# Performance work log

Measured on AMD Instinct MI355X. Metric: run time of the kernel, lower is better.

Reference implementation:

```python
import jax, jax.numpy as jnp
import numpy as np

N_NODES = 50000
N_EDGES = 800000
IN_DIM = 256
OUT_DIM = 64
HEADS = 4
NEG_SLOPE = 0.2  # PyG GATConv default


def setup_inputs() -> dict:
    key = jax.random.key(0)
    k_x, k_e, k_w, k_as, k_ad = jax.random.split(key, 5)
    x = jax.random.normal(k_x, (N_NODES, IN_DIM), dtype=jnp.float32)
    edge_index = jax.random.randint(k_e, (2, N_EDGES), 0, N_NODES, dtype=jnp.int64)
    # Glorot-ish scaled params (as in PyG GATConv)
    W = jax.random.normal(k_w, (IN_DIM, HEADS * OUT_DIM), dtype=jnp.float32) / np.sqrt(IN_DIM)
    att_src = jax.random.normal(k_as, (HEADS, OUT_DIM), dtype=jnp.float32) / np.sqrt(OUT_DIM)
    att_dst = jax.random.normal(k_ad, (HEADS, OUT_DIM), dtype=jnp.float32) / np.sqrt(OUT_DIM)
    bias = jnp.zeros((HEADS * OUT_DIM,), dtype=jnp.float32)
    return {"x": x, "edge_index": edge_index, "W": W,
            "att_src": att_src, "att_dst": att_dst, "bias": bias}


def reference(x, edge_index, W, att_src, att_dst, bias):
    N = x.shape[0]
    H, C = att_src.shape
    # add self-loops (PyG GATConv default add_self_loops=True)
    loop = jnp.arange(N, dtype=edge_index.dtype)
    src = jnp.concatenate([edge_index[0], loop])  # [E+N] message sources j
    dst = jnp.concatenate([edge_index[1], loop])  # [E+N] message targets i

    xh = (x @ W).reshape(N, H, C)                 # [N, H, C]
    a_src = jnp.einsum('nhc,hc->nh', xh, att_src)  # [N, H]
    a_dst = jnp.einsum('nhc,hc->nh', xh, att_dst)  # [N, H]

    logits = jax.nn.leaky_relu(a_src[src] + a_dst[dst], NEG_SLOPE)  # [E+N, H]
    # segment softmax over incoming edges of each destination node
    seg_max = jax.ops.segment_max(logits, dst, num_segments=N)      # [N, H]
    e = jnp.exp(logits - seg_max[dst])
    seg_sum = jax.ops.segment_sum(e, dst, num_segments=N)           # [N, H]
    alpha = e / seg_sum[dst]                                        # [E+N, H]

    # weighted scatter-aggregate of source features
    msgs = alpha[:, :, None] * xh[src]                              # [E+N, H, C]
    out = jax.ops.segment_sum(msgs, dst, num_segments=N)            # [N, H, C]
    out = out.reshape(N, H * C) + bias                              # concat heads + bias
    # h.dim() == 2 here, so the original's mean(dim=1) branch is not taken
    return out
```

## Files before the change

### kernel.cpp

```cpp
#include <hip/hip_runtime.h>

#define NEG_SLOPE 0.2f
#define LRELU(x) ((x) > 0.0f ? (x) : NEG_SLOPE * (x))

typedef short short8 __attribute__((ext_vector_type(8)));
typedef unsigned short ushort8 __attribute__((ext_vector_type(8)));
typedef float f32x4v __attribute__((ext_vector_type(4)));

__device__ __forceinline__ unsigned short f2bf(float f) {
  unsigned int u = __float_as_uint(f);
  unsigned int r = (u + 0x7FFFu + ((u >> 16) & 1u)) >> 16;
  return (unsigned short)r;
}

__device__ __forceinline__ float bf2f(unsigned short u) {
  return __uint_as_float(((unsigned int)u) << 16);
}

__device__ __forceinline__ void gload_lds16(const void* g, void* l) {
  __builtin_amdgcn_global_load_lds(
      (const __attribute__((address_space(1))) unsigned int*)g,
      (__attribute__((address_space(3))) unsigned int*)l, 16, 0, 0);
}

#define CBX 1536
#define CBC 512
#define CBW 64
#define CBF 512

__global__ __launch_bounds__(256) void fused_pre(
    const float* __restrict__ X, unsigned short* __restrict__ Xb,
    const float* __restrict__ W, unsigned short* __restrict__ Wtb,
    const int* __restrict__ ei, int* __restrict__ deg,
    int totalX, int validX, int E) {
  int b = blockIdx.x;
  int tid = threadIdx.x;
  if (b < CBX) {
    for (int i = (b * 256 + tid) * 4; i < totalX; i += CBX * 256 * 4) {
      ushort4 o;
      if (i < validX) {
        float4 v = *reinterpret_cast<const float4*>(X + i);
        o.x = f2bf(v.x); o.y = f2bf(v.y); o.z = f2bf(v.z); o.w = f2bf(v.w);
      } else {
        o.x = o.y = o.z = o.w = 0;
      }
      *reinterpret_cast<ushort4*>(Xb + i) = o;
    }
  } else if (b < CBX + CBC) {
    int bb = b - CBX;
    for (int e = bb * 256 + tid; e < E; e += CBC * 256)
      atomicAdd(&deg[ei[E + e]], 1);
  } else {
    int bb = b - CBX - CBC;
    for (int idx = bb * 256 + tid; idx < 256 * 256; idx += CBW * 256) {
      int n = idx >> 8, k = idx & 255;
      Wtb[n * 256 + k] = f2bf(W[k * 256 + n]);
    }
  }
}

__global__ __launch_bounds__(1024) void scan1_kernel(const int* __restrict__ deg,
                                                     int* __restrict__ row_start,
                                                     int* __restrict__ bsum, int N) {
  __shared__ int buf[1024];
  int i = blockIdx.x * 1024 + (int)threadIdx.x;
  int v = (i < N) ? deg[i] : 0;
  buf[threadIdx.x] = v;
  __syncthreads();
  int run = v;
  for (int off = 1; off < 1024; off <<= 1) {
    int t = ((int)threadIdx.x >= off) ? buf[threadIdx.x - off] : 0;
    __syncthreads();
    run += t;
    buf[threadIdx.x] = run;
    __syncthreads();
  }
  if (i < N) row_start[i] = run - v;
  if (threadIdx.x == 1023) bsum[blockIdx.x] = run;
}

__global__ __launch_bounds__(1024) void scan_off(int* __restrict__ row_start,
                                                 const int* __restrict__ bsum,
                                                 int nb, int N) {
  __shared__ int s_off;
  int b = blockIdx.x;
  if (threadIdx.x < 64) {
    int acc = 0;
    for (int j = (int)threadIdx.x; j < b; j += 64) acc += bsum[j];
    for (int off = 32; off; off >>= 1) acc += __shfl_down(acc, off, 64);
    if (threadIdx.x == 0) s_off = acc;
  }
  __syncthreads();
  int off = s_off;
  int i = b * 1024 + (int)threadIdx.x;
  if (i < N) row_start[i] += off;
  if (b == nb - 1 && threadIdx.x == 0) row_start[N] = off + bsum[b];
}

__global__ __launch_bounds__(256) void fused_main(
    const unsigned short* __restrict__ Xb, const unsigned short* __restrict__ Wtb,
    const float* __restrict__ attS, const float* __restrict__ attD,
    unsigned short* __restrict__ XHb, float* __restrict__ a_src,
    float* __restrict__ a_dst,
    const int* __restrict__ ei, const int* __restrict__ row_start,
    int* __restrict__ cursor, int* __restrict__ csr_src,
    int nGemm, int E, int N) {
  __shared__ unsigned short lA[128 * 32];
  __shared__ unsigned short lB[128 * 32];
  const int bid = blockIdx.x;
  const int tid = threadIdx.x;

  if (bid >= nGemm) {
    int bb = bid - nGemm;
    for (int e = bb * 256 + tid; e < E; e += CBF * 256) {
      int d = ei[E + e];
      int slot = row_start[d] + atomicAdd(&cursor[d], 1);
      csr_src[slot] = ei[e];
    }
    return;
  }

  const int lane = tid & 63;
  const int wave = tid >> 6;
  const int n0 = (bid & 1) * 128;
  const int m0 = (bid >> 1) * 128;
  const int wr = (wave >> 1) * 64;
  const int wc = (wave & 1) * 64;

  f32x4v acc[4][4];
#pragma unroll
  for (int i = 0; i < 4; ++i)
#pragma unroll
    for (int j = 0; j < 4; ++j) acc[i][j] = (f32x4v)(0.0f);

  const int srow = tid >> 2;
  const int skb = (tid & 3) * 16;
  const char* XbC = (const char*)Xb;
  const char* WtC = (const char*)Wtb;
  char* lAc = (char*)&lA[0];
  char* lBc = (char*)&lB[0];
  const int ldsB0 = wave * 1024;
  const int lr = lane & 15;
  const int hq = lane >> 4;
  const int kq = hq * 16;

  for (int k0 = 0; k0 < 256; k0 += 32) {
    const size_t kbyte = (size_t)k0 * 2 + skb;
    gload_lds16(XbC + (size_t)(m0 + srow) * 512 + kbyte, lAc + ldsB0);
    gload_lds16(XbC + (size_t)(m0 + srow + 64) * 512 + kbyte, lAc + ldsB0 + 4096);
    gload_lds16(WtC + (size_t)(n0 + srow) * 512 + kbyte, lBc + ldsB0);
    gload_lds16(WtC + (size_t)(n0 + srow + 64) * 512 + kbyte, lBc + ldsB0 + 4096);
    __syncthreads();

    short8 a[4], b[4];
#pragma unroll
    for (int i = 0; i < 4; ++i)
      a[i] = *reinterpret_cast<const short8*>(lAc + (wr + i * 16 + lr) * 64 + kq);
#pragma unroll
    for (int j = 0; j < 4; ++j)
      b[j] = *reinterpret_cast<const short8*>(lBc + (wc + j * 16 + lr) * 64 + kq);
#pragma unroll
    for (int i = 0; i < 4; ++i)
#pragma unroll
      for (int j = 0; j < 4; ++j)
        acc[i][j] = __builtin_amdgcn_mfma_f32_16x16x32_bf16(a[i], b[j], acc[i][j], 0, 0, 0);
    __syncthreads();
  }

  const int h = (n0 + wc) >> 6;
  float ws_[4], wd_[4];
#pragma unroll
  for (int j = 0; j < 4; ++j) {
    ws_[j] = attS[h * 64 + j * 16 + lr];
    wd_[j] = attD[h * 64 + j * 16 + lr];
  }
  const int rbase = m0 + wr + hq * 4;

#pragma unroll
  for (int i = 0; i < 4; ++i) {
#pragma unroll
    for (int r = 0; r < 4; ++r) {
      float ps = 0.f, pd = 0.f;
#pragma unroll
      for (int j = 0; j < 4; ++j) {
        ps += acc[i][j][r] * ws_[j];
        pd += acc[i][j][r] * wd_[j];
      }
#pragma unroll
      for (int off = 1; off < 16; off <<= 1) {
        ps += __shfl_xor(ps, off, 64);
        pd += __shfl_xor(pd, off, 64);
      }
      int row = rbase + i * 16 + r;
      if (lr == 0 && row < N) {
        a_src[row * 4 + h] = ps;
        a_dst[row * 4 + h] = pd;
      }
    }
  }

#pragma unroll
  for (int i = 0; i < 4; ++i)
#pragma unroll
    for (int j = 0; j < 4; ++j) {
      int col = n0 + wc + j * 16 + lr;
#pragma unroll
      for (int r = 0; r < 4; ++r)
        XHb[(size_t)(rbase + i * 16 + r) * 256 + col] = f2bf(acc[i][j][r]);
    }
}

__global__ __launch_bounds__(256) void gat_agg(
    const unsigned short* __restrict__ XHb, const float* __restrict__ a_src,
    const float* __restrict__ a_dst, const int* __restrict__ row_start,
    const int* __restrict__ csr_src, const float* __restrict__ bias,
    float* __restrict__ out, int N) {
  int wid = threadIdx.x >> 6;
  int lane = threadIdx.x & 63;
  int node = blockIdx.x * 4 + wid;
  if (node >= N) return;

  const int half = lane >> 5;
  const int l5 = lane & 31;
  const int h = l5 >> 3;
  const int c = l5 << 3;
  const unsigned short* __restrict__ xrow = XHb + c;

  float ad_h = a_dst[node * 4 + h];
  float as_h = a_src[node * 4 + h];

  int start = row_start[node];
  int end = row_start[node + 1];

  float acc[8];
  float sw = 0.f;
  if (half == 0) {
    float wself = __expf(LRELU(as_h + ad_h));
    ushort8 sv = *reinterpret_cast<const ushort8*>(xrow + (size_t)node * 256);
#pragma unroll
    for (int k = 0; k < 8; ++k) acc[k] = wself * bf2f(sv[k]);
    sw = wself;
  } else {
#pragma unroll
    for (int k = 0; k < 8; ++k) acc[k] = 0.f;
  }

  int p = start;
  for (; p + 8 <= end; p += 8) {
    int s0 = csr_src[p + half];
    int s1 = csr_src[p + 2 + half];
    int s2 = csr_src[p + 4 + half];
    int s3 = csr_src[p + 6 + half];
    float a0 = a_src[s0 * 4 + h] + ad_h;
    float a1 = a_src[s1 * 4 + h] + ad_h;
    float a2 = a_src[s2 * 4 + h] + ad_h;
    float a3 = a_src[s3 * 4 + h] + ad_h;
    ushort8 u0 = *reinterpret_cast<const ushort8*>(xrow + (size_t)s0 * 256);
    ushort8 u1 = *reinterpret_cast<const ushort8*>(xrow + (size_t)s1 * 256);
    ushort8 u2 = *reinterpret_cast<const ushort8*>(xrow + (size_t)s2 * 256);
    ushort8 u3 = *reinterpret_cast<const ushort8*>(xrow + (size_t)s3 * 256);
    float w0 = __expf(LRELU(a0));
    float w1 = __expf(LRELU(a1));
    float w2 = __expf(LRELU(a2));
    float w3 = __expf(LRELU(a3));
#pragma unroll
    for (int k = 0; k < 8; ++k) {
      acc[k] += w0 * bf2f(u0[k]);
      acc[k] += w1 * bf2f(u1[k]);
      acc[k] += w2 * bf2f(u2[k]);
      acc[k] += w3 * bf2f(u3[k]);
    }
    sw += (w0 + w1) + (w2 + w3);
  }
#pragma unroll
  for (int k = 0; k < 4; ++k) {
    int idx = p + 2 * k + half;
    if (idx < end) {
      int s = csr_src[idx];
      float aa = a_src[s * 4 + h] + ad_h;
      ushort8 u = *reinterpret_cast<const ushort8*>(xrow + (size_t)s * 256);
      float ww = __expf(LRELU(aa));
#pragma unroll
      for (int q = 0; q < 8; ++q) acc[q] += ww * bf2f(u[q]);
      sw += ww;
    }
  }

  sw += __shfl_xor(sw, 32, 64);
#pragma unroll
  for (int k = 0; k < 8; ++k) acc[k] += __shfl_xor(acc[k], 32, 64);

  if (half == 0) {
    float inv = 1.0f / sw;
    float4 b0 = *reinterpret_cast<const float4*>(bias + c);
    float4 b1 = *reinterpret_cast<const float4*>(bias + c + 4);
    float4 o0, o1;
    o0.x = acc[0] * inv + b0.x; o0.y = acc[1] * inv + b0.y;
    o0.z = acc[2] * inv + b0.z; o0.w = acc[3] * inv + b0.w;
    o1.x = acc[4] * inv + b1.x; o1.y = acc[5] * inv + b1.y;
    o1.z = acc[6] * inv + b1.z; o1.w = acc[7] * inv + b1.w;
    *reinterpret_cast<float4*>(out + (size_t)node * 256 + c) = o0;
    *reinterpret_cast<float4*>(out + (size_t)node * 256 + c + 4) = o1;
  }
}

extern "C" void kernel_launch(void* const* d_in, const int* in_sizes, int n_in,
                              void* d_out, int out_size, void* d_ws, size_t ws_size,
                              hipStream_t stream) {
  const float* x    = (const float*)d_in[0];
  const int*   ei   = (const int*)d_in[1];
  const float* Wm   = (const float*)d_in[2];
  const float* attS = (const float*)d_in[3];
  const float* attD = (const float*)d_in[4];
  const float* bias = (const float*)d_in[5];
  float* out = (float*)d_out;

  const int N = in_sizes[0] / 256;
  const int E = in_sizes[1] / 2;
  const int Mp = (N + 127) / 128 * 128;
  const int nb = (N + 1023) / 1024;

  char* w = (char*)d_ws;
  unsigned short* XHb = (unsigned short*)w;  w += (size_t)Mp * 256 * 2;
  unsigned short* Xb  = (unsigned short*)w;  w += (size_t)Mp * 256 * 2;
  unsigned short* Wtb = (unsigned short*)w;  w += (size_t)256 * 256 * 2;
  float* a_src = (float*)w;                  w += (size_t)N * 4 * 4;
  float* a_dst = (float*)w;                  w += (size_t)N * 4 * 4;
  int* deg = (int*)w;                        w += (size_t)N * 4;
  int* cursor = (int*)w;                     w += (size_t)N * 4;
  int* row_start = (int*)w;                  w += ((size_t)(N + 1) * 4 + 255) / 256 * 256;
  int* bsum = (int*)w;                       w += ((size_t)nb * 4 + 255) / 256 * 256;
  int* csr_src = (int*)w;                    w += (size_t)E * 4;

  hipMemsetAsync(deg, 0, (size_t)2 * N * 4, stream);

  fused_pre<<<CBX + CBC + CBW, 256, 0, stream>>>(x, Xb, Wm, Wtb, ei, deg,
                                                 Mp * 256, N * 256, E);

  scan1_kernel<<<nb, 1024, 0, stream>>>(deg, row_start, bsum, N);
  scan_off<<<nb, 1024, 0, stream>>>(row_start, bsum, nb, N);

  const int nGemm = 2 * (Mp / 128);
  fused_main<<<nGemm + CBF, 256, 0, stream>>>(Xb, Wtb, attS, attD, XHb, a_src, a_dst,
                                              ei, row_start, cursor, csr_src,
                                              nGemm, E, N);

  gat_agg<<<(N + 3) / 4, 256, 0, stream>>>(XHb, a_src, a_dst, row_start, csr_src,
                                           bias, out, N);
}
```

Measured before the change: 173.3 us.

## Fuse fp32-to-bf16 conversion of X into GEMM A-tile loads, retile 64x256

Drops the separate pre-pass that converted X to a bf16 workspace buffer. The GEMM now reads fp32 X directly, converts it in registers with packed bf16 conversion, and writes it to LDS, prefetching the next K slice in registers. Tiles change from 128x128 to 64 rows by full 256 columns, so each X row is read once instead of twice. This removes one full write and re-read of X, at the cost of register-path A loads and a larger B tile per block.

```diff
diff --git a/kernel.cpp b/kernel.cpp
--- a/kernel.cpp
+++ b/kernel.cpp
@@ -17,41 +17,32 @@
   return __uint_as_float(((unsigned int)u) << 16);
 }
 
+__device__ __forceinline__ unsigned int cvt_pk_bf16(float lo, float hi) {
+  unsigned int r;
+  asm("v_cvt_pk_bf16_f32 %0, %1, %2" : "=v"(r) : "v"(lo), "v"(hi));
+  return r;
+}
+
 __device__ __forceinline__ void gload_lds16(const void* g, void* l) {
   __builtin_amdgcn_global_load_lds(
       (const __attribute__((address_space(1))) unsigned int*)g,
       (__attribute__((address_space(3))) unsigned int*)l, 16, 0, 0);
 }
 
-#define CBX 1536
-#define CBC 512
+#define CBC 448
 #define CBW 64
 #define CBF 512
 
 __global__ __launch_bounds__(256) void fused_pre(
-    const float* __restrict__ X, unsigned short* __restrict__ Xb,
     const float* __restrict__ W, unsigned short* __restrict__ Wtb,
-    const int* __restrict__ ei, int* __restrict__ deg,
-    int totalX, int validX, int E) {
+    const int* __restrict__ ei, int* __restrict__ deg, int E) {
   int b = blockIdx.x;
   int tid = threadIdx.x;
-  if (b < CBX) {
-    for (int i = (b * 256 + tid) * 4; i < totalX; i += CBX * 256 * 4) {
-      ushort4 o;
-      if (i < validX) {
-        float4 v = *reinterpret_cast<const float4*>(X + i);
-        o.x = f2bf(v.x); o.y = f2bf(v.y); o.z = f2bf(v.z); o.w = f2bf(v.w);
-      } else {
-        o.x = o.y = o.z = o.w = 0;
-      }
-      *reinterpret_cast<ushort4*>(Xb + i) = o;
-    }
-  } else if (b < CBX + CBC) {
-    int bb = b - CBX;
-    for (int e = bb * 256 + tid; e < E; e += CBC * 256)
+  if (b < CBC) {
+    for (int e = b * 256 + tid; e < E; e += CBC * 256)
       atomicAdd(&deg[ei[E + e]], 1);
   } else {
-    int bb = b - CBX - CBC;
+    int bb = b - CBC;
     for (int idx = bb * 256 + tid; idx < 256 * 256; idx += CBW * 256) {
       int n = idx >> 8, k = idx & 255;
       Wtb[n * 256 + k] = f2bf(W[k * 256 + n]);
@@ -97,16 +88,16 @@
   if (b == nb - 1 && threadIdx.x == 0) row_start[N] = off + bsum[b];
 }
 
-__global__ __launch_bounds__(256) void fused_main(
-    const unsigned short* __restrict__ Xb, const unsigned short* __restrict__ Wtb,
+__global__ __launch_bounds__(256, 3) void fused_main(
+    const float* __restrict__ Xf, const unsigned short* __restrict__ Wtb,
     const float* __restrict__ attS, const float* __restrict__ attD,
     unsigned short* __restrict__ XHb, float* __restrict__ a_src,
     float* __restrict__ a_dst,
     const int* __restrict__ ei, const int* __restrict__ row_start,
     int* __restrict__ cursor, int* __restrict__ csr_src,
     int nGemm, int E, int N) {
-  __shared__ unsigned short lA[128 * 32];
-  __shared__ unsigned short lB[128 * 32];
+  __shared__ unsigned short lA[64 * 32];
+  __shared__ unsigned short lB[256 * 32];
   const int bid = blockIdx.x;
   const int tid = threadIdx.x;
 
@@ -122,92 +113,116 @@
 
   const int lane = tid & 63;
   const int wave = tid >> 6;
-  const int n0 = (bid & 1) * 128;
-  const int m0 = (bid >> 1) * 128;
-  const int wr = (wave >> 1) * 64;
+  const int m0 = bid * 64;
+  const int wrow = (wave >> 1) * 32;
   const int wc = (wave & 1) * 64;
 
-  f32x4v acc[4][4];
-#pragma unroll
-  for (int i = 0; i < 4; ++i)
-#pragma unroll
-    for (int j = 0; j < 4; ++j) acc[i][j] = (f32x4v)(0.0f);
+  f32x4v acc[2][8];
+#pragma unroll
+  for (int i = 0; i < 2; ++i)
+#pragma unroll
+    for (int j = 0; j < 8; ++j) acc[i][j] = (f32x4v)(0.0f);
 
   const int srow = tid >> 2;
   const int skb = (tid & 3) * 16;
-  const char* XbC = (const char*)Xb;
+  const int arow = tid >> 2;
+  const int acol = (tid & 3) * 8;
+  const float* aptr = Xf + (size_t)min(m0 + arow, N - 1) * 256 + acol;
+
   const char* WtC = (const char*)Wtb;
   char* lAc = (char*)&lA[0];
   char* lBc = (char*)&lB[0];
-  const int ldsB0 = wave * 1024;
+  const int ldsW = wave * 1024;
   const int lr = lane & 15;
   const int hq = lane >> 4;
-  const int kq = hq * 16;
-
-  for (int k0 = 0; k0 < 256; k0 += 32) {
-    const size_t kbyte = (size_t)k0 * 2 + skb;
-    gload_lds16(XbC + (size_t)(m0 + srow) * 512 + kbyte, lAc + ldsB0);
-    gload_lds16(XbC + (size_t)(m0 + srow + 64) * 512 + kbyte, lAc + ldsB0 + 4096);
-    gload_lds16(WtC + (size_t)(n0 + srow) * 512 + kbyte, lBc + ldsB0);
-    gload_lds16(WtC + (size_t)(n0 + srow + 64) * 512 + kbyte, lBc + ldsB0 + 4096);
+
+  float4 nv0 = *reinterpret_cast<const float4*>(aptr);
+  float4 nv1 = *reinterpret_cast<const float4*>(aptr + 4);
+
+#pragma unroll
+  for (int kk = 0; kk < 8; ++kk) {
+    const int k0 = kk * 32;
+#pragma unroll
+    for (int is = 0; is < 4; ++is)
+      gload_lds16(WtC + (size_t)(is * 64 + srow) * 512 + (size_t)k0 * 2 + skb,
+                  lBc + is * 4096 + ldsW);
+    {
+      uint4 wv;
+      wv.x = cvt_pk_bf16(nv0.x, nv0.y);
+      wv.y = cvt_pk_bf16(nv0.z, nv0.w);
+      wv.z = cvt_pk_bf16(nv1.x, nv1.y);
+      wv.w = cvt_pk_bf16(nv1.z, nv1.w);
+      *reinterpret_cast<uint4*>(lAc + arow * 64 + (tid & 3) * 16) = wv;
+    }
+    if (kk < 7) {
+      nv0 = *reinterpret_cast<const float4*>(aptr + k0 + 32);
+      nv1 = *reinterpret_cast<const float4*>(aptr + k0 + 36);
+    }
     __syncthreads();
 
-    short8 a[4], b[4];
-#pragma unroll
-    for (int i = 0; i < 4; ++i)
-      a[i] = *reinterpret_cast<const short8*>(lAc + (wr + i * 16 + lr) * 64 + kq);
-#pragma unroll
-    for (int j = 0; j < 4; ++j)
-      b[j] = *reinterpret_cast<const short8*>(lBc + (wc + j * 16 + lr) * 64 + kq);
-#pragma unroll
-    for (int i = 0; i < 4; ++i)
+    short8 a[2];
+#pragma unroll
+    for (int i = 0; i < 2; ++i)
+      a[i] = *reinterpret_cast<const short8*>(lAc + (wrow + i * 16 + lr) * 64 + hq * 16);
+#pragma unroll
+    for (int half = 0; half < 2; ++half) {
+      short8 b[4];
 #pragma unroll
       for (int j = 0; j < 4; ++j)
-        acc[i][j] = __builtin_amdgcn_mfma_f32_16x16x32_bf16(a[i], b[j], acc[i][j], 0, 0, 0);
+        b[j] = *reinterpret_cast<const short8*>(
+            lBc + (half * 128 + wc + j * 16 + lr) * 64 + hq * 16);
+#pragma unroll
+      for (int i = 0; i < 2; ++i)
+#pragma unroll
+        for (int j = 0; j < 4; ++j)
+          acc[i][half * 4 + j] =
+              __builtin_amdgcn_mfma_f32_16x16x32_bf16(a[i], b[j], acc[i][half * 4 + j], 0, 0, 0);
+    }
     __syncthreads();
   }
 
-  const int h = (n0 + wc) >> 6;
-  float ws_[4], wd_[4];
-#pragma unroll
-  for (int j = 0; j < 4; ++j) {
-    ws_[j] = attS[h * 64 + j * 16 + lr];
-    wd_[j] = attD[h * 64 + j * 16 + lr];
-  }
-  const int rbase = m0 + wr + hq * 4;
-
-#pragma unroll
-  for (int i = 0; i < 4; ++i) {
-#pragma unroll
-    for (int r = 0; r < 4; ++r) {
-      float ps = 0.f, pd = 0.f;
+  const int rbase = m0 + wrow + hq * 4;
+#pragma unroll
+  for (int half = 0; half < 2; ++half) {
+    const int h = half * 2 + (wave & 1);
+    float ws_[4], wd_[4];
+#pragma unroll
+    for (int j = 0; j < 4; ++j) {
+      ws_[j] = attS[h * 64 + j * 16 + lr];
+      wd_[j] = attD[h * 64 + j * 16 + lr];
+    }
+#pragma unroll
+    for (int i = 0; i < 2; ++i) {
+#pragma unroll
+      for (int r = 0; r < 4; ++r) {
+        float ps = 0.f, pd = 0.f;
+#pragma unroll
+        for (int j = 0; j < 4; ++j) {
+          ps += acc[i][half * 4 + j][r] * ws_[j];
+          pd += acc[i][half * 4 + j][r] * wd_[j];
+        }
+#pragma unroll
+        for (int off = 1; off < 16; off <<= 1) {
+          ps += __shfl_xor(ps, off, 64);
+          pd += __shfl_xor(pd, off, 64);
+        }
+        int row = rbase + i * 16 + r;
+        if (lr == 0 && row < N) {
+          a_src[row * 4 + h] = ps;
+          a_dst[row * 4 + h] = pd;
+        }
+      }
+    }
+#pragma unroll
+    for (int i = 0; i < 2; ++i)
 #pragma unroll
       for (int j = 0; j < 4; ++j) {
-        ps += acc[i][j][r] * ws_[j];
-        pd += acc[i][j][r] * wd_[j];
+        int col = half * 128 + wc + j * 16 + lr;
+#pragma unroll
+        for (int r = 0; r < 4; ++r)
+          XHb[(size_t)(rbase + i * 16 + r) * 256 + col] = f2bf(acc[i][half * 4 + j][r]);
       }
-#pragma unroll
-      for (int off = 1; off < 16; off <<= 1) {
-        ps += __shfl_xor(ps, off, 64);
-        pd += __shfl_xor(pd, off, 64);
-      }
-      int row = rbase + i * 16 + r;
-      if (lr == 0 && row < N) {
-        a_src[row * 4 + h] = ps;
-        a_dst[row * 4 + h] = pd;
-      }
-    }
-  }
-
-#pragma unroll
-  for (int i = 0; i < 4; ++i)
-#pragma unroll
-    for (int j = 0; j < 4; ++j) {
-      int col = n0 + wc + j * 16 + lr;
-#pragma unroll
-      for (int r = 0; r < 4; ++r)
-        XHb[(size_t)(rbase + i * 16 + r) * 256 + col] = f2bf(acc[i][j][r]);
-    }
+  }
 }
 
 __global__ __launch_bounds__(256) void gat_agg(
@@ -317,12 +332,11 @@
 
   const int N = in_sizes[0] / 256;
   const int E = in_sizes[1] / 2;
-  const int Mp = (N + 127) / 128 * 128;
+  const int Mp = (N + 63) / 64 * 64;
   const int nb = (N + 1023) / 1024;
 
   char* w = (char*)d_ws;
   unsigned short* XHb = (unsigned short*)w;  w += (size_t)Mp * 256 * 2;
-  unsigned short* Xb  = (unsigned short*)w;  w += (size_t)Mp * 256 * 2;
   unsigned short* Wtb = (unsigned short*)w;  w += (size_t)256 * 256 * 2;
   float* a_src = (float*)w;                  w += (size_t)N * 4 * 4;
   float* a_dst = (float*)w;                  w += (size_t)N * 4 * 4;
@@ -334,14 +348,13 @@
 
   hipMemsetAsync(deg, 0, (size_t)2 * N * 4, stream);
 
-  fused_pre<<<CBX + CBC + CBW, 256, 0, stream>>>(x, Xb, Wm, Wtb, ei, deg,
-                                                 Mp * 256, N * 256, E);
+  fused_pre<<<CBC + CBW, 256, 0, stream>>>(Wm, Wtb, ei, deg, E);
 
   scan1_kernel<<<nb, 1024, 0, stream>>>(deg, row_start, bsum, N);
   scan_off<<<nb, 1024, 0, stream>>>(row_start, bsum, nb, N);
 
-  const int nGemm = 2 * (Mp / 128);
-  fused_main<<<nGemm + CBF, 256, 0, stream>>>(Xb, Wtb, attS, attD, XHb, a_src, a_dst,
+  const int nGemm = Mp / 64;
+  fused_main<<<nGemm + CBF, 256, 0, stream>>>(x, Wtb, attS, attD, XHb, a_src, a_dst,
                                               ei, row_start, cursor, csr_src,
                                               nGemm, E, N);
 
```

New measurement: 167.2 us. 1.04x faster.

## Fuse fp32-to-bf16 conversion of X into the GEMM A-tile load

Applied to the files above, without the earlier changes.

Drops the separate pass that converted X to bf16 into a workspace buffer. The GEMM now reads fp32 X directly into registers, converts pairs with v_cvt_pk_bf16_f32, and writes the result to LDS, prefetching the next K slice into registers before the barrier. This removes a full write and re-read of a bf16 copy of X, plus the conversion blocks in the prologue kernel, whose degree-count block count is also cut. In exchange the GEMM reads twice as many bytes of A, clamps padded rows to the last valid row instead of zero-filling them, and uses register-staged stores rather than direct global-to-LDS loads for A.

```diff
diff --git a/kernel.cpp b/kernel.cpp
--- a/kernel.cpp
+++ b/kernel.cpp
@@ -17,41 +17,32 @@
   return __uint_as_float(((unsigned int)u) << 16);
 }
 
+__device__ __forceinline__ unsigned int cvt_pk_bf16(float lo, float hi) {
+  unsigned int r;
+  asm("v_cvt_pk_bf16_f32 %0, %1, %2" : "=v"(r) : "v"(lo), "v"(hi));
+  return r;
+}
+
 __device__ __forceinline__ void gload_lds16(const void* g, void* l) {
   __builtin_amdgcn_global_load_lds(
       (const __attribute__((address_space(1))) unsigned int*)g,
       (__attribute__((address_space(3))) unsigned int*)l, 16, 0, 0);
 }
 
-#define CBX 1536
-#define CBC 512
+#define CBC 448
 #define CBW 64
 #define CBF 512
 
 __global__ __launch_bounds__(256) void fused_pre(
-    const float* __restrict__ X, unsigned short* __restrict__ Xb,
     const float* __restrict__ W, unsigned short* __restrict__ Wtb,
-    const int* __restrict__ ei, int* __restrict__ deg,
-    int totalX, int validX, int E) {
+    const int* __restrict__ ei, int* __restrict__ deg, int E) {
   int b = blockIdx.x;
   int tid = threadIdx.x;
-  if (b < CBX) {
-    for (int i = (b * 256 + tid) * 4; i < totalX; i += CBX * 256 * 4) {
-      ushort4 o;
-      if (i < validX) {
-        float4 v = *reinterpret_cast<const float4*>(X + i);
-        o.x = f2bf(v.x); o.y = f2bf(v.y); o.z = f2bf(v.z); o.w = f2bf(v.w);
-      } else {
-        o.x = o.y = o.z = o.w = 0;
-      }
-      *reinterpret_cast<ushort4*>(Xb + i) = o;
-    }
-  } else if (b < CBX + CBC) {
-    int bb = b - CBX;
-    for (int e = bb * 256 + tid; e < E; e += CBC * 256)
+  if (b < CBC) {
+    for (int e = b * 256 + tid; e < E; e += CBC * 256)
       atomicAdd(&deg[ei[E + e]], 1);
   } else {
-    int bb = b - CBX - CBC;
+    int bb = b - CBC;
     for (int idx = bb * 256 + tid; idx < 256 * 256; idx += CBW * 256) {
       int n = idx >> 8, k = idx & 255;
       Wtb[n * 256 + k] = f2bf(W[k * 256 + n]);
@@ -98,7 +89,7 @@
 }
 
 __global__ __launch_bounds__(256) void fused_main(
-    const unsigned short* __restrict__ Xb, const unsigned short* __restrict__ Wtb,
+    const float* __restrict__ Xf, const unsigned short* __restrict__ Wtb,
     const float* __restrict__ attS, const float* __restrict__ attD,
     unsigned short* __restrict__ XHb, float* __restrict__ a_src,
     float* __restrict__ a_dst,
@@ -135,7 +126,9 @@
 
   const int srow = tid >> 2;
   const int skb = (tid & 3) * 16;
-  const char* XbC = (const char*)Xb;
+  const float* ap0 = Xf + (size_t)min(m0 + (tid >> 2), N - 1) * 256 + (tid & 3) * 8;
+  const float* ap1 = Xf + (size_t)min(m0 + 64 + (tid >> 2), N - 1) * 256 + (tid & 3) * 8;
+
   const char* WtC = (const char*)Wtb;
   char* lAc = (char*)&lA[0];
   char* lBc = (char*)&lB[0];
@@ -144,12 +137,32 @@
   const int hq = lane >> 4;
   const int kq = hq * 16;
 
-  for (int k0 = 0; k0 < 256; k0 += 32) {
-    const size_t kbyte = (size_t)k0 * 2 + skb;
-    gload_lds16(XbC + (size_t)(m0 + srow) * 512 + kbyte, lAc + ldsB0);
-    gload_lds16(XbC + (size_t)(m0 + srow + 64) * 512 + kbyte, lAc + ldsB0 + 4096);
-    gload_lds16(WtC + (size_t)(n0 + srow) * 512 + kbyte, lBc + ldsB0);
-    gload_lds16(WtC + (size_t)(n0 + srow + 64) * 512 + kbyte, lBc + ldsB0 + 4096);
+  float4 c0 = *reinterpret_cast<const float4*>(ap0);
+  float4 c1 = *reinterpret_cast<const float4*>(ap0 + 4);
+  float4 c2 = *reinterpret_cast<const float4*>(ap1);
+  float4 c3 = *reinterpret_cast<const float4*>(ap1 + 4);
+
+#pragma unroll
+  for (int kk = 0; kk < 8; ++kk) {
+    const int k0 = kk * 32;
+    gload_lds16(WtC + (size_t)(n0 + srow) * 512 + (size_t)k0 * 2 + skb, lBc + ldsB0);
+    gload_lds16(WtC + (size_t)(n0 + srow + 64) * 512 + (size_t)k0 * 2 + skb,
+                lBc + ldsB0 + 4096);
+    {
+      uint4 w0, w1;
+      w0.x = cvt_pk_bf16(c0.x, c0.y); w0.y = cvt_pk_bf16(c0.z, c0.w);
+      w0.z = cvt_pk_bf16(c1.x, c1.y); w0.w = cvt_pk_bf16(c1.z, c1.w);
+      w1.x = cvt_pk_bf16(c2.x, c2.y); w1.y = cvt_pk_bf16(c2.z, c2.w);
+      w1.z = cvt_pk_bf16(c3.x, c3.y); w1.w = cvt_pk_bf16(c3.z, c3.w);
+      *reinterpret_cast<uint4*>(lAc + tid * 16) = w0;
+      *reinterpret_cast<uint4*>(lAc + 4096 + tid * 16) = w1;
+    }
+    if (kk < 7) {
+      c0 = *reinterpret_cast<const float4*>(ap0 + k0 + 32);
+      c1 = *reinterpret_cast<const float4*>(ap0 + k0 + 36);
+      c2 = *reinterpret_cast<const float4*>(ap1 + k0 + 32);
+      c3 = *reinterpret_cast<const float4*>(ap1 + k0 + 36);
+    }
     __syncthreads();
 
     short8 a[4], b[4];
@@ -322,7 +335,6 @@
 
   char* w = (char*)d_ws;
   unsigned short* XHb = (unsigned short*)w;  w += (size_t)Mp * 256 * 2;
-  unsigned short* Xb  = (unsigned short*)w;  w += (size_t)Mp * 256 * 2;
   unsigned short* Wtb = (unsigned short*)w;  w += (size_t)256 * 256 * 2;
   float* a_src = (float*)w;                  w += (size_t)N * 4 * 4;
   float* a_dst = (float*)w;                  w += (size_t)N * 4 * 4;
@@ -334,14 +346,13 @@
 
   hipMemsetAsync(deg, 0, (size_t)2 * N * 4, stream);
 
-  fused_pre<<<CBX + CBC + CBW, 256, 0, stream>>>(x, Xb, Wm, Wtb, ei, deg,
-                                                 Mp * 256, N * 256, E);
+  fused_pre<<<CBC + CBW, 256, 0, stream>>>(Wm, Wtb, ei, deg, E);
 
   scan1_kernel<<<nb, 1024, 0, stream>>>(deg, row_start, bsum, N);
   scan_off<<<nb, 1024, 0, stream>>>(row_start, bsum, nb, N);
 
   const int nGemm = 2 * (Mp / 128);
-  fused_main<<<nGemm + CBF, 256, 0, stream>>>(Xb, Wtb, attS, attD, XHb, a_src, a_dst,
+  fused_main<<<nGemm + CBF, 256, 0, stream>>>(x, Wtb, attS, attD, XHb, a_src, a_dst,
                                               ei, row_start, cursor, csr_src,
                                               nGemm, E, N);
 
```

Result: no change. 174.5 us (+0.7%).
